# Optimization experiments

Measured on AMD Instinct MI355X. Metric: run time of the kernel, lower is better.

Reference implementation:

```python
import jax, jax.numpy as jnp
import numpy as np

N = 50000
E = 800000
D = 128
L = 2


def setup_inputs() -> dict:
    key = jax.random.key(0)
    k0, k1, k2 = jax.random.split(key, 3)
    x = jax.random.normal(k0, (N, D), dtype=jnp.float32)
    edge_index = jax.random.randint(k1, (2, E), 0, N, dtype=jnp.int64)
    # GCNConv weights: one [D, D] matrix + bias per layer (dim_in -> dim_in)
    W = jax.random.normal(k2, (L, D, D), dtype=jnp.float32) * (1.0 / np.sqrt(D))
    b = jnp.zeros((L, D), dtype=jnp.float32)
    return {"x": x, "edge_index": edge_index, "W": W, "b": b}


def reference(x, edge_index, W, b):
    """Stacked GCNConv + relu (dropout is identity in eval mode).

    GCNConv: out = D^{-1/2} (A + I) D^{-1/2} (X W) + b, with self-loops added.
    """
    n = x.shape[0]
    loops = jnp.arange(n, dtype=edge_index.dtype)
    src = jnp.concatenate([edge_index[0], loops])  # [E + N]
    dst = jnp.concatenate([edge_index[1], loops])  # [E + N]
    # Degree (with self-loops) based symmetric normalization
    deg = jax.ops.segment_sum(jnp.ones_like(dst, dtype=x.dtype), dst, num_segments=n)
    dinv = jax.lax.rsqrt(deg)  # deg >= 1 thanks to self-loops
    coef = (dinv[src] * dinv[dst])[:, None]  # [E + N, 1]

    num_layers = W.shape[0]
    for i in range(num_layers):
        h = x @ W[i]  # transform first, as PyG GCNConv does
        x = jax.ops.segment_sum(h[src] * coef, dst, num_segments=n) + b[i]
        x = jax.nn.relu(x)
        # F.dropout with training=False is identity
    return x
```

## Files before the change

### kernel.cpp

```cpp
#include <hip/hip_runtime.h>
#include <hip/hip_fp16.h>


#define D 128
#define SCAN_B 256
#define WP 136
#define ABI 6

typedef _Float16 half8 __attribute__((ext_vector_type(8)));
typedef float floatx4 __attribute__((ext_vector_type(4)));


__global__ void count_kernel(const int* __restrict__ dst, int* degInt,
                             int* __restrict__ rank, int e) {
    int i = blockIdx.x * blockDim.x + threadIdx.x;
    if (i < e) rank[i] = atomicAdd(&degInt[dst[i]], 1);
}

__global__ __launch_bounds__(SCAN_B) void scanA_kernel(const int* __restrict__ degInt,
                                                       int* __restrict__ partial, int n) {
    __shared__ int red[SCAN_B / 64];
    int tid = threadIdx.x;
    int i = blockIdx.x * SCAN_B + tid;
    int c = (i < n) ? degInt[i] : 0;
    int s = c;
    for (int off = 32; off > 0; off >>= 1) s += __shfl_down(s, off, 64);
    if ((tid & 63) == 0) red[tid >> 6] = s;
    __syncthreads();
    if (tid == 0) {
        int t = 0;
#pragma unroll
        for (int w = 0; w < SCAN_B / 64; ++w) t += red[w];
        partial[blockIdx.x] = t;
    }
}

__global__ __launch_bounds__(256) void scanB_kernel(const int* __restrict__ partial,
                                                    int* __restrict__ blockoff, int nb) {
    __shared__ int sc[256];
    int tid = threadIdx.x;
    int c = (tid < nb) ? partial[tid] : 0;
    sc[tid] = c;
    __syncthreads();
    for (int off = 1; off < 256; off <<= 1) {
        int v = (tid >= off) ? sc[tid - off] : 0;
        __syncthreads();
        sc[tid] += v;
        __syncthreads();
    }
    if (tid <= nb) blockoff[tid] = (tid == 0) ? 0 : sc[tid - 1];
}

__global__ __launch_bounds__(SCAN_B) void scanC_kernel(const int* __restrict__ degInt,
                                                       const int* __restrict__ blockoff,
                                                       int* __restrict__ row_ptr,
                                                       float* __restrict__ dinv,
                                                       int n, int nb) {
    __shared__ int sc[SCAN_B];
    int tid = threadIdx.x;
    int i = blockIdx.x * SCAN_B + tid;
    int c = (i < n) ? degInt[i] : 0;
    sc[tid] = c;
    __syncthreads();
    for (int off = 1; off < SCAN_B; off <<= 1) {
        int v = (tid >= off) ? sc[tid - off] : 0;
        __syncthreads();
        sc[tid] += v;
        __syncthreads();
    }
    if (i < n) {
        int base = blockoff[blockIdx.x] + sc[tid] - c;
        row_ptr[i] = base;
        dinv[i] = rsqrtf((float)(c + 1));
    }
    if (blockIdx.x == 0 && tid == 0) row_ptr[n] = blockoff[nb];
}

__global__ void fill_kernel(const int* __restrict__ src, const int* __restrict__ dst,
                            const int* __restrict__ rank,
                            const int* __restrict__ row_ptr,
                            const float* __restrict__ dinv,
                            int2* __restrict__ recs, int e) {
    int i = blockIdx.x * blockDim.x + threadIdx.x;
    if (i < e) {
        int d = dst[i];
        int s = src[i];
        int pos = row_ptr[d] + rank[i];
        int2 rec;
        rec.x = s;
        rec.y = __float_as_int(dinv[s] * dinv[d]);
        recs[pos] = rec;
    }
}

__global__ __launch_bounds__(256) void cvtw_kernel(const float* __restrict__ W,
                                                   __half* __restrict__ WhT) {
    int id = blockIdx.x * blockDim.x + threadIdx.x;
    int l = id >> 14;
    int rem = id & 16383;
    int f = rem >> 7;
    int k = rem & 127;
    WhT[id] = __float2half(W[l * 16384 + k * 128 + f]);
}


__global__ __launch_bounds__(256) void gemm_mfma_kernel(const float* __restrict__ Xf,
                                                        const __half* __restrict__ Xh,
                                                        const __half* __restrict__ WhT,
                                                        __half* __restrict__ Hh, int n,
                                                        int fromFloat) {
    __shared__ _Float16 wlds[128 * WP];
    const int tid = threadIdx.x;

#pragma unroll
    for (int q = 0; q < 8; ++q) {
        int idx = tid + q * 256;
        int row = idx >> 4;
        int col8 = (idx & 15) * 8;
        const uint2* gsrc = (const uint2*)(WhT + row * 128 + col8);
        uint2 a = gsrc[0];
        uint2 b = gsrc[1];
        uint2* ldst = (uint2*)(wlds + row * WP + col8);
        ldst[0] = a;
        ldst[1] = b;
    }
    __syncthreads();

    const int wave = tid >> 6;
    const int lane = tid & 63;
    const int m = lane & 15;
    const int quad = lane >> 4;

    const int node = blockIdx.x * 64 + wave * 16 + m;
    const int node_ld = node < n ? node : (n - 1);

    half8 bfr[4];
    if (fromFloat) {
#pragma unroll
        for (int k = 0; k < 4; ++k) {
            const float4* p = (const float4*)(Xf + (size_t)node_ld * 128 + k * 32 + quad * 8);
            float4 lo = p[0];
            float4 hi = p[1];
            half8 h;
            h[0] = (_Float16)lo.x; h[1] = (_Float16)lo.y;
            h[2] = (_Float16)lo.z; h[3] = (_Float16)lo.w;
            h[4] = (_Float16)hi.x; h[5] = (_Float16)hi.y;
            h[6] = (_Float16)hi.z; h[7] = (_Float16)hi.w;
            bfr[k] = h;
        }
    } else {
#pragma unroll
        for (int k = 0; k < 4; ++k) {
            bfr[k] = *(const half8*)(Xh + (size_t)node_ld * 128 + k * 32 + quad * 8);
        }
    }

    floatx4 acc[8];
#pragma unroll
    for (int f = 0; f < 8; ++f) acc[f] = (floatx4){0.f, 0.f, 0.f, 0.f};

#pragma unroll
    for (int f = 0; f < 8; ++f) {
#pragma unroll
        for (int k = 0; k < 4; ++k) {
            half8 a = *(const half8*)(wlds + (f * 16 + m) * WP + k * 32 + quad * 8);
            acc[f] = __builtin_amdgcn_mfma_f32_16x16x32_f16(a, bfr[k], acc[f], 0, 0, 0);
        }
    }

    if (node < n) {
#pragma unroll
        for (int f = 0; f < 8; ++f) {
            __half2 p0 = __floats2half2_rn(acc[f][0], acc[f][1]);
            __half2 p1 = __floats2half2_rn(acc[f][2], acc[f][3]);
            uint2 pk;
            pk.x = *(unsigned int*)&p0;
            pk.y = *(unsigned int*)&p1;
            *(uint2*)(Hh + (size_t)node * 128 + f * 16 + quad * 4) = pk;
        }
    }
}


__device__ inline void unpack8(uint4 u, float* f) {
    union { unsigned int x; __half2 h; } a, b, c, d;
    a.x = u.x; b.x = u.y; c.x = u.z; d.x = u.w;
    float2 f0 = __half22float2(a.h);
    float2 f1 = __half22float2(b.h);
    float2 f2 = __half22float2(c.h);
    float2 f3 = __half22float2(d.h);
    f[0] = f0.x; f[1] = f0.y; f[2] = f1.x; f[3] = f1.y;
    f[4] = f2.x; f[5] = f2.y; f[6] = f3.x; f[7] = f3.y;
}

__global__ __launch_bounds__(256) void agg_kernel(const __half* __restrict__ H,
                                                  const int2* __restrict__ recs,
                                                  const int* __restrict__ row_ptr,
                                                  const float* __restrict__ dinv,
                                                  const float* __restrict__ bias,
                                                  float* __restrict__ YF,
                                                  __half* __restrict__ YH,
                                                  int n, int writeHalf) {
    int wave = threadIdx.x >> 6;
    int lane = threadIdx.x & 63;
    int v = blockIdx.x * 4 + wave;
    if (v >= n) return;

    const int qw = lane >> 4;
    const int fl = lane & 15;
    const uint4* H16 = (const uint4*)H;

    float acc[8];
    {
        float di = dinv[v];
        float selfc = (qw == 0) ? di * di : 0.f;
        uint4 hv = H16[(size_t)v * 16 + fl];
        float f[8]; unpack8(hv, f);
#pragma unroll
        for (int t = 0; t < 8; ++t) acc[t] = f[t] * selfc;
    }

    int e0 = row_ptr[v];
    int e1 = row_ptr[v + 1];
    int e = e0;
    for (; e + 4 * ABI <= e1; e += 4 * ABI) {
        int2 r[ABI]; uint4 hu[ABI];
#pragma unroll
        for (int j = 0; j < ABI; ++j) r[j] = recs[e + 4 * j + qw];
#pragma unroll
        for (int j = 0; j < ABI; ++j) hu[j] = H16[(size_t)r[j].x * 16 + fl];
#pragma unroll
        for (int j = 0; j < ABI; ++j) {
            float c = __int_as_float(r[j].y);
            float f[8]; unpack8(hu[j], f);
#pragma unroll
            for (int t = 0; t < 8; ++t) acc[t] = fmaf(f[t], c, acc[t]);
        }
    }
    if (e < e1) {
        int2 r[ABI]; uint4 hu[ABI]; bool act[ABI];
#pragma unroll
        for (int j = 0; j < ABI; ++j) {
            int idx = e + 4 * j + qw;
            act[j] = idx < e1;
            if (act[j]) r[j] = recs[idx];
        }
#pragma unroll
        for (int j = 0; j < ABI; ++j) {
            if (act[j]) hu[j] = H16[(size_t)r[j].x * 16 + fl];
        }
#pragma unroll
        for (int j = 0; j < ABI; ++j) {
            if (act[j]) {
                float c = __int_as_float(r[j].y);
                float f[8]; unpack8(hu[j], f);
#pragma unroll
                for (int t = 0; t < 8; ++t) acc[t] = fmaf(f[t], c, acc[t]);
            }
        }
    }

#pragma unroll
    for (int t = 0; t < 8; ++t) {
        acc[t] += __shfl_xor(acc[t], 16);
        acc[t] += __shfl_xor(acc[t], 32);
    }

    if (qw == 0) {
        const float4* B4 = (const float4*)bias;
        float4 b0 = B4[fl * 2];
        float4 b1 = B4[fl * 2 + 1];
        float o[8];
        o[0] = fmaxf(acc[0] + b0.x, 0.f);
        o[1] = fmaxf(acc[1] + b0.y, 0.f);
        o[2] = fmaxf(acc[2] + b0.z, 0.f);
        o[3] = fmaxf(acc[3] + b0.w, 0.f);
        o[4] = fmaxf(acc[4] + b1.x, 0.f);
        o[5] = fmaxf(acc[5] + b1.y, 0.f);
        o[6] = fmaxf(acc[6] + b1.z, 0.f);
        o[7] = fmaxf(acc[7] + b1.w, 0.f);
        if (writeHalf) {
            __half2 p0 = __floats2half2_rn(o[0], o[1]);
            __half2 p1 = __floats2half2_rn(o[2], o[3]);
            __half2 p2 = __floats2half2_rn(o[4], o[5]);
            __half2 p3 = __floats2half2_rn(o[6], o[7]);
            uint4 pk;
            pk.x = *(unsigned int*)&p0;
            pk.y = *(unsigned int*)&p1;
            pk.z = *(unsigned int*)&p2;
            pk.w = *(unsigned int*)&p3;
            ((uint4*)YH)[(size_t)v * 16 + fl] = pk;
        } else {
            float4* Y4 = (float4*)YF;
            Y4[(size_t)v * 32 + fl * 2]     = make_float4(o[0], o[1], o[2], o[3]);
            Y4[(size_t)v * 32 + fl * 2 + 1] = make_float4(o[4], o[5], o[6], o[7]);
        }
    }
}


extern "C" void kernel_launch(void* const* d_in, const int* in_sizes, int n_in,
                              void* d_out, int out_size, void* d_ws, size_t ws_size,
                              hipStream_t stream) {
    const float* x = (const float*)d_in[0];
    const int* ei = (const int*)d_in[1];
    const float* W = (const float*)d_in[2];
    const float* b = (const float*)d_in[3];
    float* out = (float*)d_out;

    const int N = in_sizes[0] / D;
    const int E = in_sizes[1] / 2;

    const int* src = ei;
    const int* dst = ei + E;

    int* wsi = (int*)d_ws;
    float* wsf = (float*)d_ws;
    const size_t o_deg  = 0;
    const size_t o_dinv = o_deg + 50000;
    const size_t o_rp   = o_dinv + 50000;
    const size_t o_part = o_rp + 50016;
    const size_t o_boff = o_part + 256;
    const size_t o_rank = o_boff + 256;
    const size_t o_rec  = o_rank + 800000;
    const size_t o_h    = o_rec + 1600000;
    const size_t o_wht  = o_h + 3200000;
    const size_t o_y1h  = o_wht + 16384;

    int* degInt  = wsi + o_deg;
    float* dinv  = wsf + o_dinv;
    int* row_ptr = wsi + o_rp;
    int* partial = wsi + o_part;
    int* blockoff= wsi + o_boff;
    int* rank    = wsi + o_rank;
    int2* recs   = (int2*)(wsi + o_rec);
    __half* h    = (__half*)(wsi + o_h);
    __half* wht  = (__half*)(wsi + o_wht);
    __half* y1h  = (__half*)(wsi + o_y1h);

    const int nb_e = (E + 255) / 256;
    const int nb_s = (N + SCAN_B - 1) / SCAN_B;

    hipMemsetAsync(degInt, 0, (size_t)50000 * sizeof(int), stream);
    count_kernel<<<nb_e, 256, 0, stream>>>(dst, degInt, rank, E);
    scanA_kernel<<<nb_s, SCAN_B, 0, stream>>>(degInt, partial, N);
    scanB_kernel<<<1, 256, 0, stream>>>(partial, blockoff, nb_s);
    scanC_kernel<<<nb_s, SCAN_B, 0, stream>>>(degInt, blockoff, row_ptr, dinv, N, nb_s);
    fill_kernel<<<nb_e, 256, 0, stream>>>(src, dst, rank, row_ptr, dinv, recs, E);
    cvtw_kernel<<<128, 256, 0, stream>>>(W, wht);

    const int nb_gemm = (N + 63) / 64;
    const int nb_agg  = (N + 3) / 4;

    gemm_mfma_kernel<<<nb_gemm, 256, 0, stream>>>(x, nullptr, wht, h, N, 1);
    agg_kernel<<<nb_agg, 256, 0, stream>>>(h, recs, row_ptr, dinv, b, nullptr, y1h, N, 1);
    gemm_mfma_kernel<<<nb_gemm, 256, 0, stream>>>(nullptr, y1h, wht + 16384, h, N, 0);
    agg_kernel<<<nb_agg, 256, 0, stream>>>(h, recs, row_ptr, dinv, b + D, out, nullptr, N, 0);
}
```

Measured before the change: 243.6 us.

## Merge setup kernels: fuse count+weight convert, single-pass scan, gemm+fill

Combines the degree count with the weight conversion in one launch, and replaces the three-kernel scan with one kernel in which each block recomputes its prefix base by summing all earlier degrees. It also runs the first-layer GEMM and the CSR fill as disjoint block ranges of one launch so they can overlap. This cuts the launch count from about ten to six and removes the scan dependency chain. The cost is redundant reads of the degree array in the scan (quadratic in block count, though the array is small), and the gemm+fill kernel carries the GEMM's LDS footprint for the fill blocks, which may limit their occupancy.

```diff
diff --git a/kernel.cpp b/kernel.cpp
--- a/kernel.cpp
+++ b/kernel.cpp
@@ -11,35 +11,46 @@
 typedef float floatx4 __attribute__((ext_vector_type(4)));
 
 
-__global__ void count_kernel(const int* __restrict__ dst, int* degInt,
-                             int* __restrict__ rank, int e) {
-    int i = blockIdx.x * blockDim.x + threadIdx.x;
-    if (i < e) rank[i] = atomicAdd(&degInt[dst[i]], 1);
-}
-
-__global__ __launch_bounds__(SCAN_B) void scanA_kernel(const int* __restrict__ degInt,
-                                                       int* __restrict__ partial, int n) {
-    __shared__ int red[SCAN_B / 64];
+__global__ void count_cvtw_kernel(const int* __restrict__ dst, int* degInt,
+                                  int* __restrict__ rank, int e, int nbe,
+                                  const float* __restrict__ W,
+                                  __half* __restrict__ WhT) {
+    int bid = blockIdx.x;
     int tid = threadIdx.x;
-    int i = blockIdx.x * SCAN_B + tid;
+    if (bid < nbe) {
+        int i = bid * 256 + tid;
+        if (i < e) rank[i] = atomicAdd(&degInt[dst[i]], 1);
+    } else {
+        int id = (bid - nbe) * 256 + tid;
+        int l = id >> 14;
+        int rem = id & 16383;
+        int f = rem >> 7;
+        int k = rem & 127;
+        WhT[id] = __float2half(W[l * 16384 + k * 128 + f]);
+    }
+}
+
+
+__global__ __launch_bounds__(256) void scan_kernel(const int* __restrict__ degInt,
+                                                   int* __restrict__ row_ptr,
+                                                   float* __restrict__ dinv,
+                                                   int n, int nb) {
+    __shared__ int sc[256];
+    __shared__ int red[4];
+    __shared__ int base_s;
+    const int tid = threadIdx.x;
+    const int bid = blockIdx.x;
+    const int start = bid * 256;
+
+    int pre = 0;
+    for (int j = tid; j < start; j += 256) pre += degInt[j];
+    for (int off = 32; off > 0; off >>= 1) pre += __shfl_down(pre, off, 64);
+    if ((tid & 63) == 0) red[tid >> 6] = pre;
+    __syncthreads();
+    if (tid == 0) base_s = red[0] + red[1] + red[2] + red[3];
+
+    int i = start + tid;
     int c = (i < n) ? degInt[i] : 0;
-    int s = c;
-    for (int off = 32; off > 0; off >>= 1) s += __shfl_down(s, off, 64);
-    if ((tid & 63) == 0) red[tid >> 6] = s;
-    __syncthreads();
-    if (tid == 0) {
-        int t = 0;
-#pragma unroll
-        for (int w = 0; w < SCAN_B / 64; ++w) t += red[w];
-        partial[blockIdx.x] = t;
-    }
-}
-
-__global__ __launch_bounds__(256) void scanB_kernel(const int* __restrict__ partial,
-                                                    int* __restrict__ blockoff, int nb) {
-    __shared__ int sc[256];
-    int tid = threadIdx.x;
-    int c = (tid < nb) ? partial[tid] : 0;
     sc[tid] = c;
     __syncthreads();
     for (int off = 1; off < 256; off <<= 1) {
@@ -48,70 +59,21 @@
         sc[tid] += v;
         __syncthreads();
     }
-    if (tid <= nb) blockoff[tid] = (tid == 0) ? 0 : sc[tid - 1];
-}
-
-__global__ __launch_bounds__(SCAN_B) void scanC_kernel(const int* __restrict__ degInt,
-                                                       const int* __restrict__ blockoff,
-                                                       int* __restrict__ row_ptr,
-                                                       float* __restrict__ dinv,
-                                                       int n, int nb) {
-    __shared__ int sc[SCAN_B];
-    int tid = threadIdx.x;
-    int i = blockIdx.x * SCAN_B + tid;
-    int c = (i < n) ? degInt[i] : 0;
-    sc[tid] = c;
-    __syncthreads();
-    for (int off = 1; off < SCAN_B; off <<= 1) {
-        int v = (tid >= off) ? sc[tid - off] : 0;
-        __syncthreads();
-        sc[tid] += v;
-        __syncthreads();
-    }
+    int base = base_s;
     if (i < n) {
-        int base = blockoff[blockIdx.x] + sc[tid] - c;
-        row_ptr[i] = base;
+        row_ptr[i] = base + sc[tid] - c;
         dinv[i] = rsqrtf((float)(c + 1));
     }
-    if (blockIdx.x == 0 && tid == 0) row_ptr[n] = blockoff[nb];
-}
-
-__global__ void fill_kernel(const int* __restrict__ src, const int* __restrict__ dst,
-                            const int* __restrict__ rank,
-                            const int* __restrict__ row_ptr,
-                            const float* __restrict__ dinv,
-                            int2* __restrict__ recs, int e) {
-    int i = blockIdx.x * blockDim.x + threadIdx.x;
-    if (i < e) {
-        int d = dst[i];
-        int s = src[i];
-        int pos = row_ptr[d] + rank[i];
-        int2 rec;
-        rec.x = s;
-        rec.y = __float_as_int(dinv[s] * dinv[d]);
-        recs[pos] = rec;
-    }
-}
-
-__global__ __launch_bounds__(256) void cvtw_kernel(const float* __restrict__ W,
-                                                   __half* __restrict__ WhT) {
-    int id = blockIdx.x * blockDim.x + threadIdx.x;
-    int l = id >> 14;
-    int rem = id & 16383;
-    int f = rem >> 7;
-    int k = rem & 127;
-    WhT[id] = __float2half(W[l * 16384 + k * 128 + f]);
-}
-
-
-__global__ __launch_bounds__(256) void gemm_mfma_kernel(const float* __restrict__ Xf,
-                                                        const __half* __restrict__ Xh,
-                                                        const __half* __restrict__ WhT,
-                                                        __half* __restrict__ Hh, int n,
-                                                        int fromFloat) {
-    __shared__ _Float16 wlds[128 * WP];
-    const int tid = threadIdx.x;
-
+    if (bid == nb - 1 && tid == 255) row_ptr[n] = base + sc[255];
+}
+
+
+__device__ inline void gemm_body(int bid, int tid,
+                                 const float* __restrict__ Xf,
+                                 const __half* __restrict__ Xh,
+                                 const __half* __restrict__ WhT,
+                                 __half* __restrict__ Hh, int n, int fromFloat,
+                                 _Float16* wlds) {
 #pragma unroll
     for (int q = 0; q < 8; ++q) {
         int idx = tid + q * 256;
@@ -131,7 +93,7 @@
     const int m = lane & 15;
     const int quad = lane >> 4;
 
-    const int node = blockIdx.x * 64 + wave * 16 + m;
+    const int node = bid * 64 + wave * 16 + m;
     const int node_ld = node < n ? node : (n - 1);
 
     half8 bfr[4];
@@ -179,6 +141,51 @@
             *(uint2*)(Hh + (size_t)node * 128 + f * 16 + quad * 4) = pk;
         }
     }
+}
+
+__device__ inline void fill_body(int i,
+                                 const int* __restrict__ src,
+                                 const int* __restrict__ dst,
+                                 const int* __restrict__ rank,
+                                 const int* __restrict__ row_ptr,
+                                 const float* __restrict__ dinv,
+                                 int2* __restrict__ recs, int e) {
+    if (i < e) {
+        int d = dst[i];
+        int s = src[i];
+        int pos = row_ptr[d] + rank[i];
+        int2 rec;
+        rec.x = s;
+        rec.y = __float_as_int(dinv[s] * dinv[d]);
+        recs[pos] = rec;
+    }
+}
+
+
+__global__ __launch_bounds__(256) void gemmfill_kernel(const float* __restrict__ Xf,
+                                                       const __half* __restrict__ WhT,
+                                                       __half* __restrict__ Hh, int n, int nbg,
+                                                       const int* __restrict__ src,
+                                                       const int* __restrict__ dst,
+                                                       const int* __restrict__ rank,
+                                                       const int* __restrict__ row_ptr,
+                                                       const float* __restrict__ dinv,
+                                                       int2* __restrict__ recs, int e) {
+    __shared__ _Float16 wlds[128 * WP];
+    int bid = blockIdx.x;
+    int tid = threadIdx.x;
+    if (bid < nbg) {
+        gemm_body(bid, tid, Xf, nullptr, WhT, Hh, n, 1, wlds);
+    } else {
+        fill_body((bid - nbg) * 256 + tid, src, dst, rank, row_ptr, dinv, recs, e);
+    }
+}
+
+__global__ __launch_bounds__(256) void gemm_mfma_kernel(const __half* __restrict__ Xh,
+                                                        const __half* __restrict__ WhT,
+                                                        __half* __restrict__ Hh, int n) {
+    __shared__ _Float16 wlds[128 * WP];
+    gemm_body(blockIdx.x, threadIdx.x, nullptr, Xh, WhT, Hh, n, 0, wlds);
 }
 
 
@@ -319,9 +326,7 @@
     const size_t o_deg  = 0;
     const size_t o_dinv = o_deg + 50000;
     const size_t o_rp   = o_dinv + 50000;
-    const size_t o_part = o_rp + 50016;
-    const size_t o_boff = o_part + 256;
-    const size_t o_rank = o_boff + 256;
+    const size_t o_rank = o_rp + 50016;
     const size_t o_rec  = o_rank + 800000;
     const size_t o_h    = o_rec + 1600000;
     const size_t o_wht  = o_h + 3200000;
@@ -330,8 +335,6 @@
     int* degInt  = wsi + o_deg;
     float* dinv  = wsf + o_dinv;
     int* row_ptr = wsi + o_rp;
-    int* partial = wsi + o_part;
-    int* blockoff= wsi + o_boff;
     int* rank    = wsi + o_rank;
     int2* recs   = (int2*)(wsi + o_rec);
     __half* h    = (__half*)(wsi + o_h);
@@ -340,20 +343,15 @@
 
     const int nb_e = (E + 255) / 256;
     const int nb_s = (N + SCAN_B - 1) / SCAN_B;
+    const int nb_g = (N + 63) / 64;
+    const int nb_a = (N + 3) / 4;
 
     hipMemsetAsync(degInt, 0, (size_t)50000 * sizeof(int), stream);
-    count_kernel<<<nb_e, 256, 0, stream>>>(dst, degInt, rank, E);
-    scanA_kernel<<<nb_s, SCAN_B, 0, stream>>>(degInt, partial, N);
-    scanB_kernel<<<1, 256, 0, stream>>>(partial, blockoff, nb_s);
-    scanC_kernel<<<nb_s, SCAN_B, 0, stream>>>(degInt, blockoff, row_ptr, dinv, N, nb_s);
-    fill_kernel<<<nb_e, 256, 0, stream>>>(src, dst, rank, row_ptr, dinv, recs, E);
-    cvtw_kernel<<<128, 256, 0, stream>>>(W, wht);
-
-    const int nb_gemm = (N + 63) / 64;
-    const int nb_agg  = (N + 3) / 4;
-
-    gemm_mfma_kernel<<<nb_gemm, 256, 0, stream>>>(x, nullptr, wht, h, N, 1);
-    agg_kernel<<<nb_agg, 256, 0, stream>>>(h, recs, row_ptr, dinv, b, nullptr, y1h, N, 1);
-    gemm_mfma_kernel<<<nb_gemm, 256, 0, stream>>>(nullptr, y1h, wht + 16384, h, N, 0);
-    agg_kernel<<<nb_agg, 256, 0, stream>>>(h, recs, row_ptr, dinv, b + D, out, nullptr, N, 0);
-}
+    count_cvtw_kernel<<<nb_e + 128, 256, 0, stream>>>(dst, degInt, rank, E, nb_e, W, wht);
+    scan_kernel<<<nb_s, SCAN_B, 0, stream>>>(degInt, row_ptr, dinv, N, nb_s);
+    gemmfill_kernel<<<nb_g + nb_e, 256, 0, stream>>>(x, wht, h, N, nb_g,
+                                                     src, dst, rank, row_ptr, dinv, recs, E);
+    agg_kernel<<<nb_a, 256, 0, stream>>>(h, recs, row_ptr, dinv, b, nullptr, y1h, N, 1);
+    gemm_mfma_kernel<<<nb_g, 256, 0, stream>>>(y1h, wht + 16384, h, N);
+    agg_kernel<<<nb_a, 256, 0, stream>>>(h, recs, row_ptr, dinv, b + D, out, nullptr, N, 0);
+}
```

Result: slower. 256.5 us (+5.3%).
